# Kernel optimization log

Measured on AMD Instinct MI355X. Metric: run time of the kernel, lower is better.

## Reference

```python
import jax, jax.numpy as jnp
import numpy as np

B, S, D = 4, 4096, 1024
WINDOW = 129
HALF = WINDOW // 2  # 64
NEG = -1e9


def setup_inputs() -> dict:
    key = jax.random.key(0)
    ks = jax.random.split(key, 7)
    sc = 1.0 / np.sqrt(D).astype(np.float32)
    x = jax.random.normal(ks[0], (B, S, D), dtype=jnp.float32)
    Wq = jax.random.normal(ks[1], (D, D), dtype=jnp.float32) * sc
    Wk = jax.random.normal(ks[2], (D, D), dtype=jnp.float32) * sc
    Wv = jax.random.normal(ks[3], (D, D), dtype=jnp.float32) * sc
    bq = jax.random.normal(ks[4], (D,), dtype=jnp.float32) * 0.01
    bk = jax.random.normal(ks[5], (D,), dtype=jnp.float32) * 0.01
    bv = jax.random.normal(ks[6], (D,), dtype=jnp.float32) * 0.01
    return {"x": x, "Wq": Wq, "bq": bq, "Wk": Wk, "bk": bk, "Wv": Wv, "bv": bv}


def reference(x, Wq, bq, Wk, bk, Wv, bv):
    # Linear projections (torch Linear: x @ W.T + b)
    Q = x @ Wq.T + bq  # [B,S,D]
    K = x @ Wk.T + bk
    V = x @ Wv.T + bv
    # Banded additive mask: 0 inside |i-j|<=HALF, -1e9 outside
    idx = jnp.arange(S)
    mask = jnp.where(jnp.abs(idx[:, None] - idx[None, :]) <= HALF, 0.0, NEG).astype(x.dtype)
    scale = jnp.sqrt(jnp.asarray(D, dtype=x.dtype))
    scores = jnp.einsum('bqd,bkd->bqk', Q, K) / scale + mask  # [B,S,S]
    attn_weights = jax.nn.softmax(scores, axis=-1)
    output = jnp.einsum('bqk,bkd->bqd', attn_weights, V)  # [B,S,D]
    return (output, attn_weights)
```

## Files before the change

### kernel.cpp

```cpp
#include <hip/hip_runtime.h>
#include <stdint.h>

#define B_ 4
#define S_ 4096
#define D_ 1024
#define HALF_ 64

typedef __attribute__((ext_vector_type(4))) float f32x4;
typedef __attribute__((ext_vector_type(8))) short short8;
typedef __attribute__((ext_vector_type(4))) short short4v;
typedef __attribute__((ext_vector_type(4))) float float4v;

__device__ __forceinline__ short f2bf(float f) {
  union { float f; uint32_t u; } x;
  x.f = f;
  uint32_t u = x.u;
  uint32_t r = (u + 0x7FFFu + ((u >> 16) & 1u)) >> 16;
  return (short)(r & 0xFFFFu);
}

__device__ __forceinline__ void gload_lds16(const void* g, void* l) {
  __builtin_amdgcn_global_load_lds(
      (const __attribute__((address_space(1))) void*)g,
      (__attribute__((address_space(3))) void*)l, 16, 0, 0);
}

__global__ __launch_bounds__(256) void cast_f32_to_bf16(
    const float* __restrict__ in, short* __restrict__ out, int n4) {
  int stride = gridDim.x * blockDim.x;
  for (int i = blockIdx.x * blockDim.x + threadIdx.x; i < n4; i += stride) {
    float4v v = *(const float4v*)(in + (size_t)i * 4);
    short4v o;
    o.x = f2bf(v.x);
    o.y = f2bf(v.y);
    o.z = f2bf(v.z);
    o.w = f2bf(v.w);
    *(short4v*)(out + (size_t)i * 4) = o;
  }
}

__global__ __launch_bounds__(256) void gemm_bias_bf16(
    const short* __restrict__ A, const short* __restrict__ Bw,
    const float* __restrict__ bias, short* __restrict__ C,
    int M, int N, int K) {
  __shared__ __align__(16) short Asm[128 * 64];
  __shared__ __align__(16) short Bsm[128 * 64];
  const int tid = threadIdx.x;
  const int l = tid & 63;
  const int w = tid >> 6;
  const int nt = N >> 7;
  const int m0 = (blockIdx.x / nt) << 7;
  const int n0 = (blockIdx.x % nt) << 7;
  const int wr = w >> 1, wc = w & 1;

  f32x4 acc[4][4];
#pragma unroll
  for (int i = 0; i < 4; ++i)
#pragma unroll
    for (int j = 0; j < 4; ++j) acc[i][j] = (f32x4){0.f, 0.f, 0.f, 0.f};

  int srow[4], scol[4], slds[4];
#pragma unroll
  for (int r = 0; r < 4; ++r) {
    int q = r * 4096 + w * 1024 + l * 16;
    srow[r] = q >> 7;
    scol[r] = (q & 127) >> 1;
    slds[r] = (r * 4096 + w * 1024) >> 1;
  }

  const int kiters = K >> 6;
  for (int kt = 0; kt < kiters; ++kt) {
    const int kb = kt << 6;
#pragma unroll
    for (int r = 0; r < 4; ++r) {
      gload_lds16(A + (size_t)(m0 + srow[r]) * K + kb + scol[r], &Asm[slds[r]]);
      gload_lds16(Bw + (size_t)(n0 + srow[r]) * K + kb + scol[r], &Bsm[slds[r]]);
    }
    __syncthreads();
#pragma unroll
    for (int ks = 0; ks < 2; ++ks) {
      short8 af[4], bf[4];
#pragma unroll
      for (int mi = 0; mi < 4; ++mi)
        af[mi] = *(const short8*)&Asm[((wr << 6) + (mi << 4) + (l & 15)) * 64 +
                                      (ks << 5) + ((l >> 4) << 3)];
#pragma unroll
      for (int ni = 0; ni < 4; ++ni)
        bf[ni] = *(const short8*)&Bsm[((wc << 6) + (ni << 4) + (l & 15)) * 64 +
                                      (ks << 5) + ((l >> 4) << 3)];
#pragma unroll
      for (int mi = 0; mi < 4; ++mi)
#pragma unroll
        for (int ni = 0; ni < 4; ++ni)
          acc[mi][ni] = __builtin_amdgcn_mfma_f32_16x16x32_bf16(
              af[mi], bf[ni], acc[mi][ni], 0, 0, 0);
    }
    __syncthreads();
  }

#pragma unroll
  for (int ni = 0; ni < 4; ++ni) {
    const int col = n0 + (wc << 6) + (ni << 4) + (l & 15);
    const float bv = bias[col];
#pragma unroll
    for (int mi = 0; mi < 4; ++mi) {
      const int row = m0 + (wr << 6) + (mi << 4) + ((l >> 4) << 2);
#pragma unroll
      for (int r = 0; r < 4; ++r)
        C[(size_t)(row + r) * N + col] = f2bf(acc[mi][ni][r] + bv);
    }
  }
}

__global__ __launch_bounds__(256) void transpose_bf16(
    const short* __restrict__ V, short* __restrict__ Vt) {
  __shared__ __align__(16) short t[64][72];
  const int i0 = blockIdx.x << 6;
  const int d0 = blockIdx.y << 6;
  const int b = blockIdx.z;
  const int tid = threadIdx.x;
  const int lr = tid >> 3;
  const int lc = (tid & 7) << 3;
#pragma unroll
  for (int rr = 0; rr < 2; ++rr) {
    int row = (rr << 5) + lr;
    short8 v = *(const short8*)&V[((size_t)b * S_ + i0 + row) * D_ + d0 + lc];
    *(short8*)&t[row][lc] = v;
  }
  __syncthreads();
#pragma unroll
  for (int rr = 0; rr < 2; ++rr) {
    int drow = (rr << 5) + lr;
    short8 v;
#pragma unroll
    for (int q = 0; q < 8; ++q) v[q] = t[lc + q][drow];
    *(short8*)&Vt[((size_t)b * D_ + d0 + drow) * S_ + i0 + lc] = v;
  }
}

__global__ __launch_bounds__(256, 1) void swa_fused(
    const short* __restrict__ Qb, const short* __restrict__ Kb,
    const short* __restrict__ Vtb, float* __restrict__ outO,
    float* __restrict__ outW) {
  __shared__ __align__(16) short P_lds[4][16][200];
  const int tid = threadIdx.x;
  const int l = tid & 63;
  const int w = tid >> 6;
  const int b = blockIdx.y;
  const int i0 = blockIdx.x << 6;
  const int iw = i0 + (w << 4);
  const int j0 = i0 - 64;
  const int lq = l & 15;
  const int lg = l >> 4;

  f32x4 acc[12];
#pragma unroll
  for (int jc = 0; jc < 12; ++jc) acc[jc] = (f32x4){0.f, 0.f, 0.f, 0.f};

  const short* qptr = Qb + ((size_t)b * S_ + iw + lq) * D_ + (lg << 3);
  const short* kptr[12];
#pragma unroll
  for (int jc = 0; jc < 12; ++jc) {
    int j = j0 + (jc << 4) + lq;
    int jcl = j < 0 ? 0 : (j > S_ - 1 ? S_ - 1 : j);
    kptr[jc] = Kb + ((size_t)b * S_ + jcl) * D_ + (lg << 3);
  }
#pragma unroll 2
  for (int d0 = 0; d0 < D_; d0 += 32) {
    short8 qa = *(const short8*)(qptr + d0);
#pragma unroll
    for (int jc = 0; jc < 12; ++jc) {
      short8 kv = *(const short8*)(kptr[jc] + d0);
      acc[jc] = __builtin_amdgcn_mfma_f32_16x16x32_bf16(qa, kv, acc[jc], 0, 0, 0);
    }
  }

  const float scale = 0.03125f;
#pragma unroll
  for (int r = 0; r < 4; ++r) {
    const int i = iw + (lg << 2) + r;
    float sv[12];
    float m = -3.0e38f;
#pragma unroll
    for (int jc = 0; jc < 12; ++jc) {
      int j = j0 + (jc << 4) + lq;
      bool valid = (j >= i - HALF_) && (j <= i + HALF_) && (j >= 0) && (j < S_);
      float s = acc[jc][r] * scale;
      sv[jc] = valid ? s : -3.0e38f;
      m = fmaxf(m, sv[jc]);
    }
#pragma unroll
    for (int mk = 1; mk <= 8; mk <<= 1) m = fmaxf(m, __shfl_xor(m, mk, 64));
    float p[12];
    float sum = 0.f;
#pragma unroll
    for (int jc = 0; jc < 12; ++jc) {
      p[jc] = (sv[jc] > -1.0e38f) ? __expf(sv[jc] - m) : 0.f;
      sum += p[jc];
    }
#pragma unroll
    for (int mk = 1; mk <= 8; mk <<= 1) sum += __shfl_xor(sum, mk, 64);
    const float inv = 1.0f / sum;
    float* wrow = outW + ((size_t)b * S_ + i) * S_;
#pragma unroll
    for (int jc = 0; jc < 12; ++jc) {
      int j = j0 + (jc << 4) + lq;
      float pw = p[jc] * inv;
      if (j >= 0 && j < S_) wrow[j] = pw;
      P_lds[w][(lg << 2) + r][(jc << 4) + lq] = f2bf(pw);
    }
  }

  __syncthreads();

  short8 pa[6];
#pragma unroll
  for (int ks = 0; ks < 6; ++ks)
    pa[ks] = *(const short8*)&P_lds[w][lq][(ks << 5) + (lg << 3)];

  const short* vbase = Vtb + ((size_t)b * D_ + lq) * S_;
  int joff[6];
#pragma unroll
  for (int ks = 0; ks < 6; ++ks) {
    int j = j0 + (ks << 5) + (lg << 3);
    joff[ks] = j < 0 ? 0 : (j > S_ - 8 ? S_ - 8 : j);
  }
  float* obase = outO + ((size_t)b * S_ + iw + (lg << 2)) * D_ + lq;
#pragma unroll 2
  for (int dc = 0; dc < 64; ++dc) {
    f32x4 o = (f32x4){0.f, 0.f, 0.f, 0.f};
    const short* vd = vbase + ((size_t)(dc << 4)) * S_;
#pragma unroll
    for (int ks = 0; ks < 6; ++ks) {
      short8 vv = *(const short8*)(vd + joff[ks]);
      o = __builtin_amdgcn_mfma_f32_16x16x32_bf16(pa[ks], vv, o, 0, 0, 0);
    }
#pragma unroll
    for (int r = 0; r < 4; ++r) obase[(size_t)r * D_ + (dc << 4)] = o[r];
  }
}

extern "C" void kernel_launch(void* const* d_in, const int* in_sizes, int n_in,
                              void* d_out, int out_size, void* d_ws, size_t ws_size,
                              hipStream_t stream) {
  (void)in_sizes; (void)n_in; (void)out_size; (void)ws_size;
  const float* x  = (const float*)d_in[0];
  const float* Wq = (const float*)d_in[1];
  const float* bq = (const float*)d_in[2];
  const float* Wk = (const float*)d_in[3];
  const float* bk = (const float*)d_in[4];
  const float* Wv = (const float*)d_in[5];
  const float* bv = (const float*)d_in[6];

  const size_t NX = (size_t)B_ * S_ * D_;
  const size_t NW = (size_t)D_ * D_;

  char* ws = (char*)d_ws;
  size_t off = 0;
  short* xb  = (short*)(ws + off); off += NX * 2;
  short* Wqb = (short*)(ws + off); off += NW * 2;
  short* Wkb = (short*)(ws + off); off += NW * 2;
  short* Wvb = (short*)(ws + off); off += NW * 2;
  short* Qb  = (short*)(ws + off); off += NX * 2;
  short* Kb  = (short*)(ws + off); off += NX * 2;
  short* Vb  = (short*)(ws + off); off += NX * 2;
  short* Vtb = (short*)(ws + off); off += NX * 2;

  float* outO = (float*)d_out;
  float* outW = outO + NX;

  hipMemsetAsync(outW, 0, (size_t)B_ * S_ * S_ * sizeof(float), stream);

  cast_f32_to_bf16<<<4096, 256, 0, stream>>>(x, xb, (int)(NX / 4));
  cast_f32_to_bf16<<<1024, 256, 0, stream>>>(Wq, Wqb, (int)(NW / 4));
  cast_f32_to_bf16<<<1024, 256, 0, stream>>>(Wk, Wkb, (int)(NW / 4));
  cast_f32_to_bf16<<<1024, 256, 0, stream>>>(Wv, Wvb, (int)(NW / 4));

  const int M = B_ * S_, N = D_, K = D_;
  dim3 ggrid((M / 128) * (N / 128));
  gemm_bias_bf16<<<ggrid, 256, 0, stream>>>(xb, Wqb, bq, Qb, M, N, K);
  gemm_bias_bf16<<<ggrid, 256, 0, stream>>>(xb, Wkb, bk, Kb, M, N, K);
  gemm_bias_bf16<<<ggrid, 256, 0, stream>>>(xb, Wvb, bv, Vb, M, N, K);

  transpose_bf16<<<dim3(S_ / 64, D_ / 64, B_), 256, 0, stream>>>(Vb, Vtb);

  swa_fused<<<dim3(S_ / 64, B_), 256, 0, stream>>>(Qb, Kb, Vtb, outO, outW);
}
```

Before: 663.2 us.

## Fuse QKV projections into one packed GEMM and zero attention weights in-kernel

Concatenates Wq/Wk/Wv and the three biases so a single GEMM writes a packed [M,3072] QKV buffer, replacing three separate GEMM launches. The transpose and attention kernels now index into this packed layout. The full memset of the 256MB attention-weight output is removed, and the attention kernel instead zeroes the out-of-band columns of its own rows. This cuts one large redundant write pass and extra launches, but the packed layout gives strided rows for the Q/K reads and adds a small bias-packing kernel.

```diff
diff --git a/kernel.cpp b/kernel.cpp
--- a/kernel.cpp
+++ b/kernel.cpp
@@ -5,6 +5,7 @@
 #define S_ 4096
 #define D_ 1024
 #define HALF_ 64
+#define NPACK 3072
 
 typedef __attribute__((ext_vector_type(4))) float f32x4;
 typedef __attribute__((ext_vector_type(8))) short short8;
@@ -37,6 +38,14 @@
     o.w = f2bf(v.w);
     *(short4v*)(out + (size_t)i * 4) = o;
   }
+}
+
+__global__ __launch_bounds__(256) void pack_bias(
+    const float* __restrict__ bq, const float* __restrict__ bk,
+    const float* __restrict__ bv, float* __restrict__ out) {
+  int i = blockIdx.x * blockDim.x + threadIdx.x;
+  const float* src = (i < 1024) ? bq : ((i < 2048) ? bk : bv);
+  out[i] = src[i & 1023];
 }
 
 __global__ __launch_bounds__(256) void gemm_bias_bf16(
@@ -112,8 +121,8 @@
   }
 }
 
-__global__ __launch_bounds__(256) void transpose_bf16(
-    const short* __restrict__ V, short* __restrict__ Vt) {
+__global__ __launch_bounds__(256) void transpose_v_packed(
+    const short* __restrict__ QKV, short* __restrict__ Vt) {
   __shared__ __align__(16) short t[64][72];
   const int i0 = blockIdx.x << 6;
   const int d0 = blockIdx.y << 6;
@@ -124,7 +133,8 @@
 #pragma unroll
   for (int rr = 0; rr < 2; ++rr) {
     int row = (rr << 5) + lr;
-    short8 v = *(const short8*)&V[((size_t)b * S_ + i0 + row) * D_ + d0 + lc];
+    short8 v = *(const short8*)&QKV[((size_t)b * S_ + i0 + row) * NPACK + 2048 +
+                                    d0 + lc];
     *(short8*)&t[row][lc] = v;
   }
   __syncthreads();
@@ -139,9 +149,8 @@
 }
 
 __global__ __launch_bounds__(256, 1) void swa_fused(
-    const short* __restrict__ Qb, const short* __restrict__ Kb,
-    const short* __restrict__ Vtb, float* __restrict__ outO,
-    float* __restrict__ outW) {
+    const short* __restrict__ QKV, const short* __restrict__ Vtb,
+    float* __restrict__ outO, float* __restrict__ outW) {
   __shared__ __align__(16) short P_lds[4][16][200];
   const int tid = threadIdx.x;
   const int l = tid & 63;
@@ -157,13 +166,13 @@
 #pragma unroll
   for (int jc = 0; jc < 12; ++jc) acc[jc] = (f32x4){0.f, 0.f, 0.f, 0.f};
 
-  const short* qptr = Qb + ((size_t)b * S_ + iw + lq) * D_ + (lg << 3);
+  const short* qptr = QKV + ((size_t)b * S_ + iw + lq) * NPACK + (lg << 3);
   const short* kptr[12];
 #pragma unroll
   for (int jc = 0; jc < 12; ++jc) {
     int j = j0 + (jc << 4) + lq;
     int jcl = j < 0 ? 0 : (j > S_ - 1 ? S_ - 1 : j);
-    kptr[jc] = Kb + ((size_t)b * S_ + jcl) * D_ + (lg << 3);
+    kptr[jc] = QKV + ((size_t)b * S_ + jcl) * NPACK + 1024 + (lg << 3);
   }
 #pragma unroll 2
   for (int d0 = 0; d0 < D_; d0 += 32) {
@@ -208,6 +217,18 @@
       float pw = p[jc] * inv;
       if (j >= 0 && j < S_) wrow[j] = pw;
       P_lds[w][(lg << 2) + r][(jc << 4) + lq] = f2bf(pw);
+    }
+  }
+
+  {
+    const int L0 = j0 < 0 ? 0 : j0;
+    const int R0 = (j0 + 192 > S_) ? S_ : (j0 + 192);
+    const float4v z4 = {0.f, 0.f, 0.f, 0.f};
+#pragma unroll 4
+    for (int rr = 0; rr < 16; ++rr) {
+      float* rowp = outW + ((size_t)b * S_ + iw + rr) * S_;
+      for (int c = l << 2; c < L0; c += 256) *(float4v*)(rowp + c) = z4;
+      for (int c = R0 + (l << 2); c < S_; c += 256) *(float4v*)(rowp + c) = z4;
     }
   }
 
@@ -254,35 +275,29 @@
 
   const size_t NX = (size_t)B_ * S_ * D_;
   const size_t NW = (size_t)D_ * D_;
+  const int M = B_ * S_;
 
   char* ws = (char*)d_ws;
   size_t off = 0;
-  short* xb  = (short*)(ws + off); off += NX * 2;
-  short* Wqb = (short*)(ws + off); off += NW * 2;
-  short* Wkb = (short*)(ws + off); off += NW * 2;
-  short* Wvb = (short*)(ws + off); off += NW * 2;
-  short* Qb  = (short*)(ws + off); off += NX * 2;
-  short* Kb  = (short*)(ws + off); off += NX * 2;
-  short* Vb  = (short*)(ws + off); off += NX * 2;
-  short* Vtb = (short*)(ws + off); off += NX * 2;
+  short* xb    = (short*)(ws + off); off += NX * 2;
+  short* Wqkvb = (short*)(ws + off); off += 3 * NW * 2;
+  float* bias3 = (float*)(ws + off); off += NPACK * sizeof(float);
+  short* QKVp  = (short*)(ws + off); off += (size_t)M * NPACK * 2;
+  short* Vtb   = (short*)(ws + off); off += NX * 2;
 
   float* outO = (float*)d_out;
   float* outW = outO + NX;
 
-  hipMemsetAsync(outW, 0, (size_t)B_ * S_ * S_ * sizeof(float), stream);
-
   cast_f32_to_bf16<<<4096, 256, 0, stream>>>(x, xb, (int)(NX / 4));
-  cast_f32_to_bf16<<<1024, 256, 0, stream>>>(Wq, Wqb, (int)(NW / 4));
-  cast_f32_to_bf16<<<1024, 256, 0, stream>>>(Wk, Wkb, (int)(NW / 4));
-  cast_f32_to_bf16<<<1024, 256, 0, stream>>>(Wv, Wvb, (int)(NW / 4));
-
-  const int M = B_ * S_, N = D_, K = D_;
-  dim3 ggrid((M / 128) * (N / 128));
-  gemm_bias_bf16<<<ggrid, 256, 0, stream>>>(xb, Wqb, bq, Qb, M, N, K);
-  gemm_bias_bf16<<<ggrid, 256, 0, stream>>>(xb, Wkb, bk, Kb, M, N, K);
-  gemm_bias_bf16<<<ggrid, 256, 0, stream>>>(xb, Wvb, bv, Vb, M, N, K);
-
-  transpose_bf16<<<dim3(S_ / 64, D_ / 64, B_), 256, 0, stream>>>(Vb, Vtb);
-
-  swa_fused<<<dim3(S_ / 64, B_), 256, 0, stream>>>(Qb, Kb, Vtb, outO, outW);
-}
+  cast_f32_to_bf16<<<1024, 256, 0, stream>>>(Wq, Wqkvb, (int)(NW / 4));
+  cast_f32_to_bf16<<<1024, 256, 0, stream>>>(Wk, Wqkvb + NW, (int)(NW / 4));
+  cast_f32_to_bf16<<<1024, 256, 0, stream>>>(Wv, Wqkvb + 2 * NW, (int)(NW / 4));
+  pack_bias<<<12, 256, 0, stream>>>(bq, bk, bv, bias3);
+
+  dim3 ggrid((M / 128) * (NPACK / 128));
+  gemm_bias_bf16<<<ggrid, 256, 0, stream>>>(xb, Wqkvb, bias3, QKVp, M, NPACK, D_);
+
+  transpose_v_packed<<<dim3(S_ / 64, D_ / 64, B_), 256, 0, stream>>>(QKVp, Vtb);
+
+  swa_fused<<<dim3(S_ / 64, B_), 256, 0, stream>>>(QKVp, Vtb, outO, outW);
+}
```

After: 669.1 us. No clear change (+0.9%).
